# Optimization experiments

Hardware: AMD Instinct MI355X
Metric: run time of the kernel (lower is better)

## Reference

```python
import jax, jax.numpy as jnp
import numpy as np
import math

B, T, C = 4, 2048, 2048
N_HEAD = 16
HEAD_DIM = C // N_HEAD

def setup_inputs() -> dict:
    key = jax.random.key(0)
    ks = jax.random.split(key, 11)
    s = 1.0 / math.sqrt(C)
    return {
        "x": jax.random.normal(ks[0], (B, T, C), dtype=jnp.float32),
        "attn_mask": jax.random.normal(ks[1], (B, 1, 1, T), dtype=jnp.float32),
        "Wq": jax.random.normal(ks[2], (C, C), dtype=jnp.float32) * s,
        "bq": jax.random.normal(ks[3], (C,), dtype=jnp.float32) * 0.02,
        "Wk": jax.random.normal(ks[4], (C, C), dtype=jnp.float32) * s,
        "bk": jax.random.normal(ks[5], (C,), dtype=jnp.float32) * 0.02,
        "Wv": jax.random.normal(ks[6], (C, C), dtype=jnp.float32) * s,
        "bv": jax.random.normal(ks[7], (C,), dtype=jnp.float32) * 0.02,
        "Wp": jax.random.normal(ks[8], (C, C), dtype=jnp.float32) * s,
        "bp": jax.random.normal(ks[9], (C,), dtype=jnp.float32) * 0.02,
    }

def reference(x, attn_mask, Wq, bq, Wk, bk, Wv, bv, Wp, bp):
    Bx, Tx, Cx = x.shape
    # QKV projections -> (B, H, T, d)
    q = (x @ Wq.T + bq).reshape(Bx, Tx, N_HEAD, HEAD_DIM).transpose(0, 2, 1, 3)
    k = (x @ Wk.T + bk).reshape(Bx, Tx, N_HEAD, HEAD_DIM).transpose(0, 2, 1, 3)
    v = (x @ Wv.T + bv).reshape(Bx, Tx, N_HEAD, HEAD_DIM).transpose(0, 2, 1, 3)
    scale = 1.0 / math.sqrt(HEAD_DIM)
    att = jnp.einsum('bhqd,bhkd->bhqk', q, k) * scale  # (B,H,T,T)
    causal = jnp.tril(jnp.ones((Tx, Tx), dtype=bool))
    att = jnp.where(causal[None, None], att, -jnp.inf)
    att = att + attn_mask  # additive broadcast mask
    att = jax.nn.softmax(att, axis=-1)
    y = jnp.einsum('bhqk,bhkd->bhqd', att, v)
    y = y.transpose(0, 2, 1, 3).reshape(Bx, Tx, Cx)
    return y @ Wp.T + bp
```

## Files before the change

### kernel.cpp

```cpp
#include <hip/hip_runtime.h>
#include <hip/hip_bf16.h>

#define G1 __attribute__((address_space(1)))
#define L3 __attribute__((address_space(3)))

typedef __bf16 bf16x8 __attribute__((ext_vector_type(8)));
typedef _Float16 half4 __attribute__((ext_vector_type(4)));
typedef float f32x4 __attribute__((ext_vector_type(4)));

__device__ __forceinline__ ushort f2bf(float f) {
  union { float f; uint u; } v; v.f = f;
  uint u = v.u;
  u += 0x7fffu + ((u >> 16) & 1u);
  return (ushort)(u >> 16);
}
__device__ __forceinline__ ushort f2h(float f) {
  _Float16 h = (_Float16)f;
  union { _Float16 h; ushort u; } v; v.h = h;
  return v.u;
}

__global__ void cast_bf16_kernel(const float* __restrict__ in, ushort* __restrict__ out, int n4) {
  int i = blockIdx.x * 256 + threadIdx.x;
  if (i >= n4) return;
  float4 v = ((const float4*)in)[i];
  ushort4 o;
  o.x = f2bf(v.x); o.y = f2bf(v.y); o.z = f2bf(v.z); o.w = f2bf(v.w);
  ((ushort4*)out)[i] = o;
}

#define STAGE_A(bf, kt) {                                                       \
    __builtin_amdgcn_global_load_lds((G1 uint*)(Ag0 + (kt) * 32),               \
        (L3 uint*)&As[bf][tid * 8], 16, 0, 0);                                  \
    __builtin_amdgcn_global_load_lds((G1 uint*)(Ag1 + (kt) * 32),               \
        (L3 uint*)&As[bf][4096 + tid * 8], 16, 0, 0);                           \
  }
#define STAGE_B(bf, kt) {                                                       \
    __builtin_amdgcn_global_load_lds((G1 uint*)(Bg0 + (kt) * 32),               \
        (L3 uint*)&Bs[bf][tid * 8], 16, 0, 0);                                  \
    __builtin_amdgcn_global_load_lds((G1 uint*)(Bg1 + (kt) * 32),               \
        (L3 uint*)&Bs[bf][4096 + tid * 8], 16, 0, 0);                           \
  }

template <int MODE>
__global__ __launch_bounds__(512, 2)
void gemm256(const ushort* __restrict__ A, const ushort* __restrict__ Bm,
             const float* __restrict__ bias, void* __restrict__ outp,
             int M, int N, int K) {
  __shared__ ushort As[4][8192];
  __shared__ ushort Bs[4][8192];
  const int tid  = threadIdx.x;
  const int wave = tid >> 6, lane = tid & 63;
  const int l15  = lane & 15, quad = lane >> 4;

  const int nwg = gridDim.x;
  const int cpx = nwg >> 3;
  const int swz = (blockIdx.x & 7) * cpx + (blockIdx.x >> 3);
  const int nbn = N >> 8;
  const int m0 = (swz / nbn) * 256;
  const int n0 = (swz % nbn) * 256;

  const int wm = (wave >> 2) << 7;
  const int wn = (wave & 3) << 6;

  const int fck = (quad ^ ((l15 >> 1) & 3)) << 3;

  const int srow = tid >> 2;
  const int sck  = ((tid & 3) ^ ((srow >> 1) & 3)) * 8;
  const ushort* Ag0 = A  + (size_t)(m0 + srow) * K + sck;
  const ushort* Ag1 = A  + (size_t)(m0 + 128 + srow) * K + sck;
  const ushort* Bg0 = Bm + (size_t)(n0 + srow) * K + sck;
  const ushort* Bg1 = Bm + (size_t)(n0 + 128 + srow) * K + sck;

  f32x4 acc[8][4] = {};

  STAGE_A(0, 0) STAGE_B(0, 0)
  STAGE_A(1, 1) STAGE_B(1, 1)
  STAGE_A(2, 2) STAGE_B(2, 2)
  asm volatile("s_waitcnt vmcnt(8)" ::: "memory");
  __builtin_amdgcn_s_barrier();

  const int NT = K >> 5;
  for (int j = 0; j < NT; j += 4) {
#pragma unroll
    for (int tt = 0; tt < 4; ++tt) {
      const int t   = j + tt;
      const int kt3 = (t + 3) & (NT - 1);
      const int b3  = (tt + 3) & 3;
      bf16x8 bfr[4], af[4];
#pragma unroll
      for (int ni = 0; ni < 4; ++ni)
        bfr[ni] = *(const bf16x8*)&Bs[tt][(wn + ni * 16 + l15) * 32 + fck];
#pragma unroll
      for (int mi = 0; mi < 4; ++mi)
        af[mi] = *(const bf16x8*)&As[tt][(wm + mi * 16 + l15) * 32 + fck];
      STAGE_A(b3, kt3)
      __builtin_amdgcn_s_barrier();
      asm volatile("s_waitcnt lgkmcnt(0)" ::: "memory");
      __builtin_amdgcn_s_setprio(1);
#pragma unroll
      for (int mi = 0; mi < 4; ++mi)
#pragma unroll
        for (int ni = 0; ni < 4; ++ni)
          acc[mi][ni] = __builtin_amdgcn_mfma_f32_16x16x32_bf16(af[mi], bfr[ni], acc[mi][ni], 0, 0, 0);
      __builtin_amdgcn_s_setprio(0);
      __builtin_amdgcn_s_barrier();
#pragma unroll
      for (int mi = 0; mi < 4; ++mi)
        af[mi] = *(const bf16x8*)&As[tt][(wm + (mi + 4) * 16 + l15) * 32 + fck];
      STAGE_B(b3, kt3)
      __builtin_amdgcn_s_barrier();
      asm volatile("s_waitcnt lgkmcnt(0)" ::: "memory");
      __builtin_amdgcn_s_setprio(1);
#pragma unroll
      for (int mi = 0; mi < 4; ++mi)
#pragma unroll
        for (int ni = 0; ni < 4; ++ni)
          acc[mi + 4][ni] = __builtin_amdgcn_mfma_f32_16x16x32_bf16(af[mi], bfr[ni], acc[mi + 4][ni], 0, 0, 0);
      __builtin_amdgcn_s_setprio(0);
      asm volatile("s_waitcnt vmcnt(8)" ::: "memory");
      __builtin_amdgcn_s_barrier();
    }
  }
  asm volatile("s_waitcnt vmcnt(0)" ::: "memory");

#pragma unroll
  for (int mi = 0; mi < 8; ++mi)
#pragma unroll
    for (int ni = 0; ni < 4; ++ni) {
      int n = n0 + wn + ni * 16 + l15;
      float bv = bias[n];
      int mbase = m0 + wm + mi * 16 + quad * 4;
      if (MODE == 1) {
        int b = mbase >> 11, t = mbase & 2047;
        int h = n >> 7, dd = n & 127;
        ushort4 o;
        o.x = f2h(acc[mi][ni][0] + bv);
        o.y = f2h(acc[mi][ni][1] + bv);
        o.z = f2h(acc[mi][ni][2] + bv);
        o.w = f2h(acc[mi][ni][3] + bv);
        *(ushort4*)&((ushort*)outp)[(((size_t)(b * 16 + h) * 128 + dd) << 11) + t] = o;
      } else {
#pragma unroll
        for (int r = 0; r < 4; ++r) {
          int m = mbase + r;
          float v = acc[mi][ni][r] + bv;
          if (MODE == 0) {
            int b = m >> 11, t = m & 2047, h = n >> 7, dd = n & 127;
            ((ushort*)outp)[(((size_t)(b * 16 + h) * 2048 + t) << 7) + dd] = f2bf(v);
          } else {
            ((float*)outp)[(size_t)m * N + n] = v;
          }
        }
      }
    }
}

__global__ __launch_bounds__(256, 2)
void attn_kernel(const ushort* __restrict__ Q, const ushort* __restrict__ Kh,
                 const ushort* __restrict__ Vt, const float* __restrict__ mask,
                 ushort* __restrict__ Y) {
  __shared__ ushort Ks[2][64 * 128];
  __shared__ ushort Vs[2][128 * 64];
  const int tid  = threadIdx.x;
  const int wave = tid >> 6, lane = tid & 63;
  const int l15  = lane & 15, quad = lane >> 4;
  const int bh = blockIdx.x;
  const int qt = 15 - blockIdx.y;
  const int b  = bh >> 4, h = bh & 15;
  const int qw0 = qt * 128 + wave * 32;
  const ushort* Qb = Q  + (size_t)bh * 2048 * 128;
  const ushort* Kb = Kh + (size_t)bh * 2048 * 128;
  const ushort* Vb = Vt + (size_t)bh * 128 * 2048;
  const float*  mrow = mask + b * 2048;

  bf16x8 aq[2][4];
#pragma unroll
  for (int q2 = 0; q2 < 2; ++q2)
#pragma unroll
    for (int dk = 0; dk < 4; ++dk)
      aq[q2][dk] = *(const bf16x8*)(Qb + (size_t)(qw0 + q2 * 16 + l15) * 128 + dk * 32 + quad * 8);

  auto stageKV = [&](int it, int bufb) {
    const int k0s = it * 64;
#pragma unroll
    for (int i = 0; i < 4; ++i) {
      int c = i * 256 + tid;
      int t = c >> 4, ckG = (c & 15) ^ (t & 15);
      __builtin_amdgcn_global_load_lds((G1 uint*)(Kb + (size_t)(k0s + t) * 128 + ckG * 8),
                                       (L3 uint*)&Ks[bufb][c * 8], 16, 0, 0);
    }
#pragma unroll
    for (int i = 0; i < 4; ++i) {
      int c = i * 256 + tid;
      int d = c >> 3, ckG = (c & 7) ^ (d & 7);
      __builtin_amdgcn_global_load_lds((G1 uint*)(Vb + (size_t)d * 2048 + k0s + ckG * 8),
                                       (L3 uint*)&Vs[bufb][c * 8], 16, 0, 0);
    }
  };

  float mi_[2], li[2];
  f32x4 OT[8][2] = {};
  mi_[0] = mi_[1] = -3.0e38f;
  li[0] = li[1] = 0.f;

  const float scale = 0.08838834764831845f;
  const int nkt = 2 * qt + 2;

  stageKV(0, 0);
  for (int it = 0; it < nkt; ++it) {
    const int k0 = it * 64;
    const int bb = it & 1;
    asm volatile("s_waitcnt vmcnt(0)" ::: "memory");
    __builtin_amdgcn_s_barrier();
    if (it + 1 < nkt) stageKV(it + 1, bb ^ 1);

    if (k0 <= qw0 + 31) {
      float4 mk[4];
#pragma unroll
      for (int ns = 0; ns < 4; ++ns)
        mk[ns] = *(const float4*)&mrow[k0 + ns * 16 + quad * 4];

      f32x4 s[2][4] = {};
#pragma unroll
      for (int ns = 0; ns < 4; ++ns) {
        bf16x8 kb[4];
#pragma unroll
        for (int dk = 0; dk < 4; ++dk) {
          int ck = ((dk * 4 + quad) ^ l15);
          kb[dk] = *(const bf16x8*)&Ks[bb][(ns * 16 + l15) * 128 + ck * 8];
        }
#pragma unroll
        for (int q2 = 0; q2 < 2; ++q2)
#pragma unroll
          for (int dk = 0; dk < 4; ++dk)
            s[q2][ns] = __builtin_amdgcn_mfma_f32_16x16x32_bf16(kb[dk], aq[q2][dk], s[q2][ns], 0, 0, 0);
      }

      half4 pf[2][4];
#pragma unroll
      for (int q2 = 0; q2 < 2; ++q2) {
        const int qr = qw0 + q2 * 16 + l15;
#pragma unroll
        for (int ns = 0; ns < 4; ++ns)
#pragma unroll
          for (int r = 0; r < 4; ++r) {
            int kc = k0 + ns * 16 + quad * 4 + r;
            float v = s[q2][ns][r] * scale + mk[ns][r];
            s[q2][ns][r] = (kc > qr) ? -3.0e38f : v;
          }
        float rm = -3.0e38f;
#pragma unroll
        for (int ns = 0; ns < 4; ++ns)
          rm = fmaxf(rm, fmaxf(fmaxf(s[q2][ns][0], s[q2][ns][1]), fmaxf(s[q2][ns][2], s[q2][ns][3])));
        rm = fmaxf(rm, __shfl_xor(rm, 16));
        rm = fmaxf(rm, __shfl_xor(rm, 32));
        float mnew = fmaxf(mi_[q2], rm);
        float al = __expf(mi_[q2] - mnew);
        float rs = 0.f;
#pragma unroll
        for (int ns = 0; ns < 4; ++ns) {
#pragma unroll
          for (int r = 0; r < 4; ++r) {
            float p = __expf(s[q2][ns][r] - mnew);
            s[q2][ns][r] = p;
            rs += p;
          }
          pf[q2][ns] = half4{(_Float16)s[q2][ns][0], (_Float16)s[q2][ns][1],
                             (_Float16)s[q2][ns][2], (_Float16)s[q2][ns][3]};
        }
        rs += __shfl_xor(rs, 16);
        rs += __shfl_xor(rs, 32);
        li[q2] = li[q2] * al + rs;
        mi_[q2] = mnew;
#pragma unroll
        for (int ddt = 0; ddt < 8; ++ddt) OT[ddt][q2] *= al;
      }

#pragma unroll
      for (int ns = 0; ns < 4; ++ns)
#pragma unroll
        for (int ddt = 0; ddt < 8; ++ddt) {
          int row = ddt * 16 + l15;
          int ck = (2 * ns + (quad >> 1)) ^ (l15 & 7);
          half4 vf = *(const half4*)&Vs[bb][row * 64 + ck * 8 + (quad & 1) * 4];
#pragma unroll
          for (int q2 = 0; q2 < 2; ++q2)
            OT[ddt][q2] = __builtin_amdgcn_mfma_f32_16x16x16f16(vf, pf[q2][ns], OT[ddt][q2], 0, 0, 0);
        }
    }
    __builtin_amdgcn_s_barrier();
  }

#pragma unroll
  for (int q2 = 0; q2 < 2; ++q2) {
    float inv = 1.0f / li[q2];
    int t = qw0 + q2 * 16 + l15;
#pragma unroll
    for (int ddt = 0; ddt < 8; ++ddt) {
      ushort4 o;
      o.x = f2bf(OT[ddt][q2][0] * inv);
      o.y = f2bf(OT[ddt][q2][1] * inv);
      o.z = f2bf(OT[ddt][q2][2] * inv);
      o.w = f2bf(OT[ddt][q2][3] * inv);
      *(ushort4*)&Y[((size_t)(b * 2048 + t)) * 2048 + h * 128 + ddt * 16 + quad * 4] = o;
    }
  }
}

extern "C" void kernel_launch(void* const* d_in, const int* in_sizes, int n_in,
                              void* d_out, int out_size, void* d_ws, size_t ws_size,
                              hipStream_t stream) {
  const float* x     = (const float*)d_in[0];
  const float* amask = (const float*)d_in[1];
  const float* Wq = (const float*)d_in[2];
  const float* bq = (const float*)d_in[3];
  const float* Wk = (const float*)d_in[4];
  const float* bk = (const float*)d_in[5];
  const float* Wv = (const float*)d_in[6];
  const float* bv = (const float*)d_in[7];
  const float* Wp = (const float*)d_in[8];
  const float* bp = (const float*)d_in[9];

  char* ws = (char*)d_ws;
  ushort* xb  = (ushort*)(ws);
  ushort* Wqb = (ushort*)(ws + 33554432);
  ushort* Wkb = (ushort*)(ws + 41943040);
  ushort* Wvb = (ushort*)(ws + 50331648);
  ushort* Wpb = (ushort*)(ws + 58720256);
  ushort* Qb  = (ushort*)(ws + 67108864);
  ushort* Kb  = (ushort*)(ws + 100663296);
  ushort* Vtb = (ushort*)(ws + 134217728);
  ushort* Yb  = (ushort*)(ws + 167772160);

  cast_bf16_kernel<<<16384, 256, 0, stream>>>(x,  xb,  4194304);
  cast_bf16_kernel<<<4096,  256, 0, stream>>>(Wq, Wqb, 1048576);
  cast_bf16_kernel<<<4096,  256, 0, stream>>>(Wk, Wkb, 1048576);
  cast_bf16_kernel<<<4096,  256, 0, stream>>>(Wv, Wvb, 1048576);
  cast_bf16_kernel<<<4096,  256, 0, stream>>>(Wp, Wpb, 1048576);

  gemm256<0><<<256, 512, 0, stream>>>(xb, Wqb, bq, Qb,  8192, 2048, 2048);
  gemm256<0><<<256, 512, 0, stream>>>(xb, Wkb, bk, Kb,  8192, 2048, 2048);
  gemm256<1><<<256, 512, 0, stream>>>(xb, Wvb, bv, Vtb, 8192, 2048, 2048);

  attn_kernel<<<dim3(64, 16), 256, 0, stream>>>(Qb, Kb, Vtb, amask, Yb);

  gemm256<2><<<256, 512, 0, stream>>>(Yb, Wpb, bp, d_out, 8192, 2048, 2048);
}
```

Before: 550.1 us.

## Fuse QKV GEMMs into one launch and retune attention softmax and tiling

```diff
diff --git a/kernel.cpp b/kernel.cpp
--- a/kernel.cpp
+++ b/kernel.cpp
@@ -7,6 +7,12 @@
 typedef __bf16 bf16x8 __attribute__((ext_vector_type(8)));
 typedef _Float16 half4 __attribute__((ext_vector_type(4)));
 typedef float f32x4 __attribute__((ext_vector_type(4)));
+
+#if __has_builtin(__builtin_amdgcn_exp2f)
+#define EXP2F(x) __builtin_amdgcn_exp2f(x)
+#else
+#define EXP2F(x) __expf((x) * 0.69314718056f)
+#endif
 
 __device__ __forceinline__ ushort f2bf(float f) {
   union { float f; uint u; } v; v.f = f;
@@ -29,6 +35,11 @@
   ((ushort4*)out)[i] = o;
 }
 
+__global__ void scale_mask_kernel(const float* __restrict__ in, float* __restrict__ out, int n) {
+  int i = blockIdx.x * 256 + threadIdx.x;
+  if (i < n) out[i] = in[i] * 1.44269504088896f;
+}
+
 #define STAGE_A(bf, kt) {                                                       \
     __builtin_amdgcn_global_load_lds((G1 uint*)(Ag0 + (kt) * 32),               \
         (L3 uint*)&As[bf][tid * 8], 16, 0, 0);                                  \
@@ -44,9 +55,13 @@
 
 template <int MODE>
 __global__ __launch_bounds__(512, 2)
-void gemm256(const ushort* __restrict__ A, const ushort* __restrict__ Bm,
-             const float* __restrict__ bias, void* __restrict__ outp,
-             int M, int N, int K) {
+void gemm256(const ushort* __restrict__ A,
+             const ushort* __restrict__ B0, const ushort* __restrict__ B1,
+             const ushort* __restrict__ B2,
+             const float* __restrict__ bias0, const float* __restrict__ bias1,
+             const float* __restrict__ bias2,
+             void* __restrict__ out0, void* __restrict__ out1, void* __restrict__ out2,
+             int nbn, int K) {
   __shared__ ushort As[4][8192];
   __shared__ ushort Bs[4][8192];
   const int tid  = threadIdx.x;
@@ -56,9 +71,18 @@
   const int nwg = gridDim.x;
   const int cpx = nwg >> 3;
   const int swz = (blockIdx.x & 7) * cpx + (blockIdx.x >> 3);
-  const int nbn = N >> 8;
   const int m0 = (swz / nbn) * 256;
-  const int n0 = (swz % nbn) * 256;
+  const int n0g = (swz % nbn) * 256;
+
+  int seg = 0, nn = n0g;
+  const ushort* Bmat = B0;
+  const float* bias = bias0;
+  if (MODE == 3) {
+    seg = n0g >> 11;
+    nn  = n0g & 2047;
+    Bmat = seg == 0 ? B0 : (seg == 1 ? B1 : B2);
+    bias = seg == 0 ? bias0 : (seg == 1 ? bias1 : bias2);
+  }
 
   const int wm = (wave >> 2) << 7;
   const int wn = (wave & 3) << 6;
@@ -67,10 +91,10 @@
 
   const int srow = tid >> 2;
   const int sck  = ((tid & 3) ^ ((srow >> 1) & 3)) * 8;
-  const ushort* Ag0 = A  + (size_t)(m0 + srow) * K + sck;
-  const ushort* Ag1 = A  + (size_t)(m0 + 128 + srow) * K + sck;
-  const ushort* Bg0 = Bm + (size_t)(n0 + srow) * K + sck;
-  const ushort* Bg1 = Bm + (size_t)(n0 + 128 + srow) * K + sck;
+  const ushort* Ag0 = A    + (size_t)(m0 + srow) * K + sck;
+  const ushort* Ag1 = A    + (size_t)(m0 + 128 + srow) * K + sck;
+  const ushort* Bg0 = Bmat + (size_t)(nn + srow) * K + sck;
+  const ushort* Bg1 = Bmat + (size_t)(nn + 128 + srow) * K + sck;
 
   f32x4 acc[8][4] = {};
 
@@ -87,92 +111,93 @@
       const int t   = j + tt;
       const int kt3 = (t + 3) & (NT - 1);
       const int b3  = (tt + 3) & 3;
-      bf16x8 bfr[4], af[4];
+      bf16x8 bfr[4], af[8];
 #pragma unroll
       for (int ni = 0; ni < 4; ++ni)
         bfr[ni] = *(const bf16x8*)&Bs[tt][(wn + ni * 16 + l15) * 32 + fck];
 #pragma unroll
-      for (int mi = 0; mi < 4; ++mi)
+      for (int mi = 0; mi < 8; ++mi)
         af[mi] = *(const bf16x8*)&As[tt][(wm + mi * 16 + l15) * 32 + fck];
-      STAGE_A(b3, kt3)
+      STAGE_A(b3, kt3) STAGE_B(b3, kt3)
       __builtin_amdgcn_s_barrier();
       asm volatile("s_waitcnt lgkmcnt(0)" ::: "memory");
       __builtin_amdgcn_s_setprio(1);
 #pragma unroll
-      for (int mi = 0; mi < 4; ++mi)
+      for (int mi = 0; mi < 8; ++mi)
 #pragma unroll
         for (int ni = 0; ni < 4; ++ni)
           acc[mi][ni] = __builtin_amdgcn_mfma_f32_16x16x32_bf16(af[mi], bfr[ni], acc[mi][ni], 0, 0, 0);
       __builtin_amdgcn_s_setprio(0);
-      __builtin_amdgcn_s_barrier();
-#pragma unroll
-      for (int mi = 0; mi < 4; ++mi)
-        af[mi] = *(const bf16x8*)&As[tt][(wm + (mi + 4) * 16 + l15) * 32 + fck];
-      STAGE_B(b3, kt3)
-      __builtin_amdgcn_s_barrier();
-      asm volatile("s_waitcnt lgkmcnt(0)" ::: "memory");
-      __builtin_amdgcn_s_setprio(1);
-#pragma unroll
-      for (int mi = 0; mi < 4; ++mi)
-#pragma unroll
-        for (int ni = 0; ni < 4; ++ni)
-          acc[mi + 4][ni] = __builtin_amdgcn_mfma_f32_16x16x32_bf16(af[mi], bfr[ni], acc[mi + 4][ni], 0, 0, 0);
-      __builtin_amdgcn_s_setprio(0);
       asm volatile("s_waitcnt vmcnt(8)" ::: "memory");
       __builtin_amdgcn_s_barrier();
     }
   }
   asm volatile("s_waitcnt vmcnt(0)" ::: "memory");
 
-#pragma unroll
-  for (int mi = 0; mi < 8; ++mi)
-#pragma unroll
-    for (int ni = 0; ni < 4; ++ni) {
-      int n = n0 + wn + ni * 16 + l15;
-      float bv = bias[n];
-      int mbase = m0 + wm + mi * 16 + quad * 4;
-      if (MODE == 1) {
-        int b = mbase >> 11, t = mbase & 2047;
-        int h = n >> 7, dd = n & 127;
+  if (MODE == 3 && seg == 2) {
+#pragma unroll
+    for (int mi = 0; mi < 8; ++mi)
+#pragma unroll
+      for (int ni = 0; ni < 4; ++ni) {
+        int n = nn + wn + ni * 16 + l15;
+        float bv = bias[n];
+        int mbase = m0 + wm + mi * 16 + quad * 4;
+        int b = mbase >> 11, tq = mbase & 2047, h = n >> 7, dd = n & 127;
         ushort4 o;
         o.x = f2h(acc[mi][ni][0] + bv);
         o.y = f2h(acc[mi][ni][1] + bv);
         o.z = f2h(acc[mi][ni][2] + bv);
         o.w = f2h(acc[mi][ni][3] + bv);
-        *(ushort4*)&((ushort*)outp)[(((size_t)(b * 16 + h) * 128 + dd) << 11) + t] = o;
-      } else {
+        *(ushort4*)&((ushort*)out2)[(((size_t)(b * 16 + h) * 128 + dd) << 11) + tq] = o;
+      }
+  } else if (MODE == 3) {
+    ushort* dst = seg == 0 ? (ushort*)out0 : (ushort*)out1;
+#pragma unroll
+    for (int mi = 0; mi < 8; ++mi)
+#pragma unroll
+      for (int ni = 0; ni < 4; ++ni) {
+        int n = nn + wn + ni * 16 + l15;
+        float bv = bias[n];
+        int mbase = m0 + wm + mi * 16 + quad * 4;
 #pragma unroll
         for (int r = 0; r < 4; ++r) {
           int m = mbase + r;
-          float v = acc[mi][ni][r] + bv;
-          if (MODE == 0) {
-            int b = m >> 11, t = m & 2047, h = n >> 7, dd = n & 127;
-            ((ushort*)outp)[(((size_t)(b * 16 + h) * 2048 + t) << 7) + dd] = f2bf(v);
-          } else {
-            ((float*)outp)[(size_t)m * N + n] = v;
-          }
-        }
-      }
-    }
-}
-
-__global__ __launch_bounds__(256, 2)
+          int b = m >> 11, tq = m & 2047, h = n >> 7, dd = n & 127;
+          dst[(((size_t)(b * 16 + h) * 2048 + tq) << 7) + dd] = f2bf(acc[mi][ni][r] + bv);
+        }
+      }
+  } else {
+#pragma unroll
+    for (int mi = 0; mi < 8; ++mi)
+#pragma unroll
+      for (int ni = 0; ni < 4; ++ni) {
+        int n = n0g + wn + ni * 16 + l15;
+        float bv = bias[n];
+        int mbase = m0 + wm + mi * 16 + quad * 4;
+#pragma unroll
+        for (int r = 0; r < 4; ++r)
+          ((float*)out0)[(size_t)(mbase + r) * 2048 + n] = acc[mi][ni][r] + bv;
+      }
+  }
+}
+
+__global__ __launch_bounds__(512, 4)
 void attn_kernel(const ushort* __restrict__ Q, const ushort* __restrict__ Kh,
-                 const ushort* __restrict__ Vt, const float* __restrict__ mask,
+                 const ushort* __restrict__ Vt, const float* __restrict__ mask2,
                  ushort* __restrict__ Y) {
-  __shared__ ushort Ks[2][64 * 128];
-  __shared__ ushort Vs[2][128 * 64];
+  __shared__ ushort Ks[2][8192];
+  __shared__ ushort Vs[2][8192];
   const int tid  = threadIdx.x;
   const int wave = tid >> 6, lane = tid & 63;
   const int l15  = lane & 15, quad = lane >> 4;
   const int bh = blockIdx.x;
-  const int qt = 15 - blockIdx.y;
+  const int qb = 7 - blockIdx.y;
   const int b  = bh >> 4, h = bh & 15;
-  const int qw0 = qt * 128 + wave * 32;
+  const int qw0 = qb * 256 + wave * 32;
   const ushort* Qb = Q  + (size_t)bh * 2048 * 128;
   const ushort* Kb = Kh + (size_t)bh * 2048 * 128;
   const ushort* Vb = Vt + (size_t)bh * 128 * 2048;
-  const float*  mrow = mask + b * 2048;
+  const float*  mrow = mask2 + b * 2048;
 
   bf16x8 aq[2][4];
 #pragma unroll
@@ -181,18 +206,18 @@
     for (int dk = 0; dk < 4; ++dk)
       aq[q2][dk] = *(const bf16x8*)(Qb + (size_t)(qw0 + q2 * 16 + l15) * 128 + dk * 32 + quad * 8);
 
-  auto stageKV = [&](int it, int bufb) {
-    const int k0s = it * 64;
-#pragma unroll
-    for (int i = 0; i < 4; ++i) {
-      int c = i * 256 + tid;
+  auto stageKV = [&](int itn, int bufb) {
+    const int k0s = itn * 64;
+#pragma unroll
+    for (int i = 0; i < 2; ++i) {
+      int c = i * 512 + tid;
       int t = c >> 4, ckG = (c & 15) ^ (t & 15);
       __builtin_amdgcn_global_load_lds((G1 uint*)(Kb + (size_t)(k0s + t) * 128 + ckG * 8),
                                        (L3 uint*)&Ks[bufb][c * 8], 16, 0, 0);
     }
 #pragma unroll
-    for (int i = 0; i < 4; ++i) {
-      int c = i * 256 + tid;
+    for (int i = 0; i < 2; ++i) {
+      int c = i * 512 + tid;
       int d = c >> 3, ckG = (c & 7) ^ (d & 7);
       __builtin_amdgcn_global_load_lds((G1 uint*)(Vb + (size_t)d * 2048 + k0s + ckG * 8),
                                        (L3 uint*)&Vs[bufb][c * 8], 16, 0, 0);
@@ -204,8 +229,8 @@
   mi_[0] = mi_[1] = -3.0e38f;
   li[0] = li[1] = 0.f;
 
-  const float scale = 0.08838834764831845f;
-  const int nkt = 2 * qt + 2;
+  const float scale2 = 0.08838834764831845f * 1.44269504088896f;
+  const int nkt = 4 * qb + 4;
 
   stageKV(0, 0);
   for (int it = 0; it < nkt; ++it) {
@@ -216,11 +241,6 @@
     if (it + 1 < nkt) stageKV(it + 1, bb ^ 1);
 
     if (k0 <= qw0 + 31) {
-      float4 mk[4];
-#pragma unroll
-      for (int ns = 0; ns < 4; ++ns)
-        mk[ns] = *(const float4*)&mrow[k0 + ns * 16 + quad * 4];
-
       f32x4 s[2][4] = {};
 #pragma unroll
       for (int ns = 0; ns < 4; ++ns) {
@@ -237,44 +257,72 @@
             s[q2][ns] = __builtin_amdgcn_mfma_f32_16x16x32_bf16(kb[dk], aq[q2][dk], s[q2][ns], 0, 0, 0);
       }
 
+      const bool dmask = (k0 + 63 > qw0);
       half4 pf[2][4];
 #pragma unroll
       for (int q2 = 0; q2 < 2; ++q2) {
         const int qr = qw0 + q2 * 16 + l15;
+        float4 mk[4];
 #pragma unroll
         for (int ns = 0; ns < 4; ++ns)
-#pragma unroll
-          for (int r = 0; r < 4; ++r) {
-            int kc = k0 + ns * 16 + quad * 4 + r;
-            float v = s[q2][ns][r] * scale + mk[ns][r];
-            s[q2][ns][r] = (kc > qr) ? -3.0e38f : v;
-          }
+          mk[ns] = *(const float4*)&mrow[k0 + ns * 16 + quad * 4];
+#pragma unroll
+        for (int ns = 0; ns < 4; ++ns)
+#pragma unroll
+          for (int r = 0; r < 4; ++r)
+            s[q2][ns][r] = fmaf(s[q2][ns][r], scale2, mk[ns][r]);
+        if (dmask) {
+#pragma unroll
+          for (int ns = 0; ns < 4; ++ns)
+#pragma unroll
+            for (int r = 0; r < 4; ++r) {
+              int kc = k0 + ns * 16 + quad * 4 + r;
+              if (kc > qr) s[q2][ns][r] = -3.0e38f;
+            }
+        }
         float rm = -3.0e38f;
 #pragma unroll
         for (int ns = 0; ns < 4; ++ns)
           rm = fmaxf(rm, fmaxf(fmaxf(s[q2][ns][0], s[q2][ns][1]), fmaxf(s[q2][ns][2], s[q2][ns][3])));
         rm = fmaxf(rm, __shfl_xor(rm, 16));
         rm = fmaxf(rm, __shfl_xor(rm, 32));
-        float mnew = fmaxf(mi_[q2], rm);
-        float al = __expf(mi_[q2] - mnew);
+        const bool skip = __all(rm <= mi_[q2] + 10.0f);
+        float mnew = mi_[q2], al = 1.0f;
+        if (!skip) {
+          mnew = fmaxf(mi_[q2], rm);
+          al = EXP2F(mi_[q2] - mnew);
+        }
         float rs = 0.f;
 #pragma unroll
         for (int ns = 0; ns < 4; ++ns) {
 #pragma unroll
           for (int r = 0; r < 4; ++r) {
-            float p = __expf(s[q2][ns][r] - mnew);
+            float p = EXP2F(s[q2][ns][r] - mnew);
             s[q2][ns][r] = p;
             rs += p;
           }
+#if __has_builtin(__builtin_amdgcn_cvt_pkrtz)
+          {
+            auto lo = __builtin_amdgcn_cvt_pkrtz(s[q2][ns][0], s[q2][ns][1]);
+            auto hi = __builtin_amdgcn_cvt_pkrtz(s[q2][ns][2], s[q2][ns][3]);
+            pf[q2][ns] = half4{(_Float16)lo[0], (_Float16)lo[1],
+                               (_Float16)hi[0], (_Float16)hi[1]};
+          }
+#else
           pf[q2][ns] = half4{(_Float16)s[q2][ns][0], (_Float16)s[q2][ns][1],
                              (_Float16)s[q2][ns][2], (_Float16)s[q2][ns][3]};
+#endif
         }
         rs += __shfl_xor(rs, 16);
         rs += __shfl_xor(rs, 32);
-        li[q2] = li[q2] * al + rs;
-        mi_[q2] = mnew;
-#pragma unroll
-        for (int ddt = 0; ddt < 8; ++ddt) OT[ddt][q2] *= al;
+        if (skip) {
+          li[q2] += rs;
+        } else {
+          li[q2] = li[q2] * al + rs;
+          mi_[q2] = mnew;
+#pragma unroll
+          for (int ddt = 0; ddt < 8; ++ddt) OT[ddt][q2] *= al;
+        }
       }
 
 #pragma unroll
@@ -332,18 +380,20 @@
   ushort* Kb  = (ushort*)(ws + 100663296);
   ushort* Vtb = (ushort*)(ws + 134217728);
   ushort* Yb  = (ushort*)(ws + 167772160);
+  float* mask2 = (float*)d_out;
 
   cast_bf16_kernel<<<16384, 256, 0, stream>>>(x,  xb,  4194304);
   cast_bf16_kernel<<<4096,  256, 0, stream>>>(Wq, Wqb, 1048576);
   cast_bf16_kernel<<<4096,  256, 0, stream>>>(Wk, Wkb, 1048576);
   cast_bf16_kernel<<<4096,  256, 0, stream>>>(Wv, Wvb, 1048576);
   cast_bf16_kernel<<<4096,  256, 0, stream>>>(Wp, Wpb, 1048576);
-
-  gemm256<0><<<256, 512, 0, stream>>>(xb, Wqb, bq, Qb,  8192, 2048, 2048);
-  gemm256<0><<<256, 512, 0, stream>>>(xb, Wkb, bk, Kb,  8192, 2048, 2048);
-  gemm256<1><<<256, 512, 0, stream>>>(xb, Wvb, bv, Vtb, 8192, 2048, 2048);
-
-  attn_kernel<<<dim3(64, 16), 256, 0, stream>>>(Qb, Kb, Vtb, amask, Yb);
-
-  gemm256<2><<<256, 512, 0, stream>>>(Yb, Wpb, bp, d_out, 8192, 2048, 2048);
-}
+  scale_mask_kernel<<<32, 256, 0, stream>>>(amask, mask2, 8192);
+
+  gemm256<3><<<768, 512, 0, stream>>>(xb, Wqb, Wkb, Wvb, bq, bk, bv,
+                                      Qb, Kb, Vtb, 24, 2048);
+
+  attn_kernel<<<dim3(64, 8), 512, 0, stream>>>(Qb, Kb, Vtb, mask2, Yb);
+
+  gemm256<2><<<256, 512, 0, stream>>>(Yb, Wpb, nullptr, nullptr, bp, nullptr, nullptr,
+                                      d_out, nullptr, nullptr, 8, 2048);
+}
```

New measurement: 845.3 us. +53.7%, slower.
